# Optimization experiments

Measured on AMD Instinct MI355X. Metric: run time of the kernel, lower is better.

Reference implementation:

```python
import jax, jax.numpy as jnp
import numpy as np

GRID_SIZE = 5
GRID_LO, GRID_HI = -1.0, 1.0


def setup_inputs() -> dict:
    key = jax.random.key(0)
    k1, k2 = jax.random.split(key)
    B, out_dim, in_dim, H, W = 8, 64, 64, 192, 192
    G = GRID_SIZE + 1
    x = jax.random.normal(k1, (B, in_dim, H, W), dtype=jnp.float32)
    coef = jax.random.normal(k2, (B, out_dim, in_dim, G), dtype=jnp.float32) * 0.1
    return {"x": x, "coef": coef}


def reference(x, coef):
    # x: [B, in_dim, H, W]; coef: [B, out_dim, in_dim, G] with G = grid_size + 1
    G = GRID_SIZE + 1
    grid = jnp.linspace(GRID_LO, GRID_HI, G, dtype=x.dtype)
    lo, hi = grid[0], grid[-1]
    spacing = grid[1] - grid[0]

    B, in_dim, H, W = x.shape
    out_dim = coef.shape[1]
    P = H * W

    xf = x.reshape(B, in_dim, P)
    xc = jnp.clip(xf, lo, hi)
    nx = (xc - lo) / spacing                      # normalized coordinate in [0, grid_size]
    idx = jnp.clip(jnp.floor(nx).astype(jnp.int32), 0, GRID_SIZE - 1)  # left knot
    frac = nx - idx.astype(x.dtype)               # fractional offset (grad flows via nx)
    w1 = 1.0 - frac
    w2 = frac
    idx_next = jnp.clip(idx + 1, 0, GRID_SIZE)    # right knot (max index = G-1)

    # Two-hot interpolation weights over the G grid points: [B, in, P, G]
    Wt = (w1[..., None] * jax.nn.one_hot(idx, G, dtype=x.dtype)
          + w2[..., None] * jax.nn.one_hot(idx_next, G, dtype=x.dtype))

    # result[b,o,p] = sum_i sum_g Wt[b,i,p,g] * coef[b,o,i,g]
    out = jnp.einsum('bipg,boig->bop', Wt, coef)
    return out.reshape(B, out_dim, H, W)
```

## Files before the change

kernel.cpp:

```cpp
#include <hip/hip_runtime.h>
#include <stdint.h>


typedef __fp16 half8_t __attribute__((ext_vector_type(8)));
typedef __fp16 half2_t __attribute__((ext_vector_type(2)));
typedef float f32x4 __attribute__((ext_vector_type(4)));

#define NBATCH 8
#define OD 64
#define ID 64
#define PIX 36864
#define NG 6
#define PT 192
#define KI 16
#define NCHUNK 4
#define KC (KI * NG)
#define AROW 392
#define PTILES (PIX / PT)

__global__ __launch_bounds__(256, 3)
void kan_mfma(const float* __restrict__ x, const float* __restrict__ coef,
              float* __restrict__ out) {
  const int t = threadIdx.x;
  const int lane = t & 63;
  const int wave = t >> 6;
  const int q8 = lane >> 4;
  const int col = lane & 15;

  const int bid = blockIdx.x;
  const int b = bid / PTILES;
  const int ptile = bid % PTILES;
  const int p0 = ptile * PT;

  __shared__ __fp16 A_lds[OD][AROW] __attribute__((aligned(16)));

  const int iof0 = (q8 & 1) * 8;
  const int ghalf = q8 >> 1;
  const float* xb = x + (size_t)b * ID * PIX + p0 + wave * 48 + col
                      + (size_t)iof0 * PIX;

  float xcur[24];
#pragma unroll
  for (int j = 0; j < 8; ++j) {
    const float* xj = xb + (size_t)j * PIX;
    xcur[j * 3 + 0] = xj[0];
    xcur[j * 3 + 1] = xj[16];
    xcur[j * 3 + 2] = xj[32];
  }

  {
    const int o = t >> 2;
    const int c = t & 3;
    const float* crow = coef + (size_t)b * (OD * ID * NG) + o * (ID * NG) + c * KC;
    __fp16* arow = &A_lds[o][c * KC];
#pragma unroll
    for (int blk = 0; blk < 8; ++blk) {
      f32x4 va = ((const f32x4*)crow)[blk * 3 + 0];
      f32x4 vb = ((const f32x4*)crow)[blk * 3 + 1];
      f32x4 vc = ((const f32x4*)crow)[blk * 3 + 2];
      const float lo[NG] = {va[0], va[1], va[2], va[3], vb[0], vb[1]};
      const float hi[NG] = {vb[2], vb[3], vc[0], vc[1], vc[2], vc[3]};
#pragma unroll
      for (int g = 0; g < NG; ++g) {
        half2_t h2 = __builtin_amdgcn_cvt_pkrtz(lo[g], hi[g]);
        *(half2_t*)&arow[g * KI + blk * 2] = h2;
      }
    }
  }

  f32x4 acc[4][3];
#pragma unroll
  for (int i = 0; i < 4; ++i)
#pragma unroll
    for (int j = 0; j < 3; ++j)
      acc[i][j] = (f32x4){0.f, 0.f, 0.f, 0.f};

  __syncthreads();

#pragma unroll
  for (int c = 0; c < NCHUNK; ++c) {
    float xnext[24];
    if (c + 1 < NCHUNK) {
      const float* xs = xb + (size_t)((c + 1) * KI) * PIX;
#pragma unroll
      for (int j = 0; j < 8; ++j) {
        const float* xj = xs + (size_t)j * PIX;
        xnext[j * 3 + 0] = xj[0];
        xnext[j * 3 + 1] = xj[16];
        xnext[j * 3 + 2] = xj[32];
      }
    }

    float nxv[3][8];
#pragma unroll
    for (int j = 0; j < 8; ++j) {
#pragma unroll
      for (int pt = 0; pt < 3; ++pt)
        nxv[pt][j] = (fminf(fmaxf(xcur[j * 3 + pt], -1.f), 1.f) + 1.f) * 2.5f;
    }

#pragma unroll
    for (int ks = 0; ks < 3; ++ks) {
      half8_t af[4];
#pragma unroll
      for (int ot = 0; ot < 4; ++ot)
        af[ot] = *(const half8_t*)&A_lds[ot * 16 + col][c * KC + ks * 32 + q8 * 8];

      const float gf = (float)(2 * ks + ghalf);
#pragma unroll
      for (int pti = 0; pti < 3; ++pti) {
        union { half2_t h2[4]; half8_t v; } bu;
#pragma unroll
        for (int jj = 0; jj < 4; ++jj) {
          float h0 = fmaxf(0.f, 1.f - fabsf(nxv[pti][2 * jj] - gf));
          float h1 = fmaxf(0.f, 1.f - fabsf(nxv[pti][2 * jj + 1] - gf));
          bu.h2[jj] = __builtin_amdgcn_cvt_pkrtz(h0, h1);
        }
#pragma unroll
        for (int ot = 0; ot < 4; ++ot)
          acc[ot][pti] = __builtin_amdgcn_mfma_f32_16x16x32_f16(
              af[ot], bu.v, acc[ot][pti], 0, 0, 0);
      }
    }

    if (c + 1 < NCHUNK) {
#pragma unroll
      for (int k = 0; k < 24; ++k) xcur[k] = xnext[k];
    }
  }

  float* ob = out + (size_t)b * OD * PIX + p0;
#pragma unroll
  for (int ot = 0; ot < 4; ++ot) {
#pragma unroll
    for (int pti = 0; pti < 3; ++pti) {
      int p = wave * 48 + pti * 16 + col;
#pragma unroll
      for (int r = 0; r < 4; ++r) {
        int o = ot * 16 + q8 * 4 + r;
        ob[(size_t)o * PIX + p] = acc[ot][pti][r];
      }
    }
  }
}

extern "C" void kernel_launch(void* const* d_in, const int* in_sizes, int n_in,
                              void* d_out, int out_size, void* d_ws, size_t ws_size,
                              hipStream_t stream) {
  const float* x = (const float*)d_in[0];
  const float* coef = (const float*)d_in[1];
  float* out = (float*)d_out;
  dim3 grid(NBATCH * PTILES);
  dim3 block(256);
  hipLaunchKernelGGL(kan_mfma, grid, block, 0, stream, x, coef, out);
}
```

Measured before the change: 157.2 us.

## Stage x through double-buffered LDS with vector loads and packed fp16 hat math

Replaces per-thread scalar strided loads of x with cooperative dwordx4 inline-asm loads into a double-buffered LDS tile of normalized coordinates, clamped once per element. The hat-function weights are now computed with packed half2 arithmetic instead of fp32 ops plus conversion. Occupancy hint drops from 3 to 2 blocks per SM because of the extra LDS and barriers per chunk. This trades redundant global loads and ALU work for LDS traffic, extra syncs and fp16 precision in the weight computation.

```diff
diff --git a/kernel.cpp b/kernel.cpp
--- a/kernel.cpp
+++ b/kernel.cpp
@@ -16,9 +16,27 @@
 #define NCHUNK 4
 #define KC (KI * NG)
 #define AROW 392
+#define XROW 200
 #define PTILES (PIX / PT)
 
-__global__ __launch_bounds__(256, 3)
+#define LOADX(dst, cc)                                                          \
+  do {                                                                          \
+    const float* a_ = xstage + (size_t)((cc) * KI + trow) * PIX;                \
+    asm volatile("global_load_dwordx4 %0, %3, off\n\t"                          \
+                 "global_load_dwordx4 %1, %3, off offset:16\n\t"                \
+                 "global_load_dwordx4 %2, %3, off offset:32"                    \
+                 : "=&v"(dst[0]), "=&v"(dst[1]), "=&v"(dst[2])                  \
+                 : "v"(a_));                                                    \
+    __builtin_amdgcn_sched_barrier(0);                                          \
+  } while (0)
+
+#define VMWAIT0                                                                 \
+  do {                                                                          \
+    asm volatile("s_waitcnt vmcnt(0)" ::: "memory");                            \
+    __builtin_amdgcn_sched_barrier(0);                                          \
+  } while (0)
+
+__global__ __launch_bounds__(256, 2)
 void kan_mfma(const float* __restrict__ x, const float* __restrict__ coef,
               float* __restrict__ out) {
   const int t = threadIdx.x;
@@ -33,20 +51,17 @@
   const int p0 = ptile * PT;
 
   __shared__ __fp16 A_lds[OD][AROW] __attribute__((aligned(16)));
+  __shared__ float nx_lds[2][KI][XROW] __attribute__((aligned(16)));
 
   const int iof0 = (q8 & 1) * 8;
   const int ghalf = q8 >> 1;
-  const float* xb = x + (size_t)b * ID * PIX + p0 + wave * 48 + col
-                      + (size_t)iof0 * PIX;
+  const int trow = t >> 4;
+  const int tc12 = (t & 15) * 12;
+  const float* xstage = x + (size_t)b * ID * PIX + p0 + tc12;
 
-  float xcur[24];
-#pragma unroll
-  for (int j = 0; j < 8; ++j) {
-    const float* xj = xb + (size_t)j * PIX;
-    xcur[j * 3 + 0] = xj[0];
-    xcur[j * 3 + 1] = xj[16];
-    xcur[j * 3 + 2] = xj[32];
-  }
+  f32x4 xr[3];
+
+  LOADX(xr, 0);
 
   {
     const int o = t >> 2;
@@ -75,28 +90,34 @@
     for (int j = 0; j < 3; ++j)
       acc[i][j] = (f32x4){0.f, 0.f, 0.f, 0.f};
 
+  VMWAIT0;
+#pragma unroll
+  for (int r = 0; r < 3; ++r) {
+    f32x4 v = xr[r];
+#pragma unroll
+    for (int e = 0; e < 4; ++e)
+      v[e] = fminf(fmaxf(v[e] * 2.5f + 2.5f, 0.f), 5.f);
+    *(f32x4*)&nx_lds[0][trow][tc12 + r * 4] = v;
+  }
   __syncthreads();
+
+  const int wp = wave * 48 + col;
+  const half2_t one2 = {(__fp16)1.f, (__fp16)1.f};
+  const half2_t zero2 = {(__fp16)0.f, (__fp16)0.f};
 
 #pragma unroll
   for (int c = 0; c < NCHUNK; ++c) {
-    float xnext[24];
-    if (c + 1 < NCHUNK) {
-      const float* xs = xb + (size_t)((c + 1) * KI) * PIX;
+    if (c + 1 < NCHUNK) LOADX(xr, c + 1);
+
+    half2_t nx2[3][4];
 #pragma unroll
-      for (int j = 0; j < 8; ++j) {
-        const float* xj = xs + (size_t)j * PIX;
-        xnext[j * 3 + 0] = xj[0];
-        xnext[j * 3 + 1] = xj[16];
-        xnext[j * 3 + 2] = xj[32];
+    for (int pti = 0; pti < 3; ++pti) {
+#pragma unroll
+      for (int jj = 0; jj < 4; ++jj) {
+        float lo = nx_lds[c & 1][iof0 + 2 * jj][wp + pti * 16];
+        float hi = nx_lds[c & 1][iof0 + 2 * jj + 1][wp + pti * 16];
+        nx2[pti][jj] = __builtin_amdgcn_cvt_pkrtz(lo, hi);
       }
-    }
-
-    float nxv[3][8];
-#pragma unroll
-    for (int j = 0; j < 8; ++j) {
-#pragma unroll
-      for (int pt = 0; pt < 3; ++pt)
-        nxv[pt][j] = (fminf(fmaxf(xcur[j * 3 + pt], -1.f), 1.f) + 1.f) * 2.5f;
     }
 
 #pragma unroll
@@ -107,14 +128,19 @@
         af[ot] = *(const half8_t*)&A_lds[ot * 16 + col][c * KC + ks * 32 + q8 * 8];
 
       const float gf = (float)(2 * ks + ghalf);
+      const __fp16 gh = (__fp16)gf;
+      const half2_t gf2 = {gh, gh};
 #pragma unroll
       for (int pti = 0; pti < 3; ++pti) {
         union { half2_t h2[4]; half8_t v; } bu;
 #pragma unroll
         for (int jj = 0; jj < 4; ++jj) {
-          float h0 = fmaxf(0.f, 1.f - fabsf(nxv[pti][2 * jj] - gf));
-          float h1 = fmaxf(0.f, 1.f - fabsf(nxv[pti][2 * jj + 1] - gf));
-          bu.h2[jj] = __builtin_amdgcn_cvt_pkrtz(h0, h1);
+          half2_t d = nx2[pti][jj] - gf2;
+          union { half2_t h; uint32_t u; } du;
+          du.h = d;
+          du.u &= 0x7FFF7FFFu;
+          half2_t hh = one2 - du.h;
+          bu.h2[jj] = __builtin_elementwise_max(hh, zero2);
         }
 #pragma unroll
         for (int ot = 0; ot < 4; ++ot)
@@ -124,8 +150,16 @@
     }
 
     if (c + 1 < NCHUNK) {
+      VMWAIT0;
 #pragma unroll
-      for (int k = 0; k < 24; ++k) xcur[k] = xnext[k];
+      for (int r = 0; r < 3; ++r) {
+        f32x4 v = xr[r];
+#pragma unroll
+        for (int e = 0; e < 4; ++e)
+          v[e] = fminf(fmaxf(v[e] * 2.5f + 2.5f, 0.f), 5.f);
+        *(f32x4*)&nx_lds[(c + 1) & 1][trow][tc12 + r * 4] = v;
+      }
+      __syncthreads();
     }
   }
 
```

Measured after the change: 144.2 us. 8.2% less time.
